# Optimization experiments

Hardware: AMD Instinct MI355X
Metric: run time of the kernel (lower is better)

Reference implementation:

```python
import jax, jax.numpy as jnp
import numpy as np

N_NODES = 1_000_000
D_IN = 128
GRAPH_STATE_DIM = 128  # node_hidden_sizes[-1] before doubling
N_GRAPHS = 4096


def setup_inputs() -> dict:
    key = jax.random.key(0)
    ks = jax.random.split(key, 10)
    s = lambda fan_in: 1.0 / np.sqrt(fan_in)
    return {
        "node_states": jax.random.normal(ks[0], (N_NODES, D_IN), dtype=jnp.float32),
        "graph_idx": jax.random.randint(ks[1], (N_NODES,), 0, N_GRAPHS),
        # MLP1: D_IN -> 64 -> 2*GRAPH_STATE_DIM
        "W1": jax.random.uniform(ks[2], (D_IN, 64), jnp.float32, -s(D_IN), s(D_IN)),
        "b1": jnp.zeros((64,), jnp.float32),
        "W2": jax.random.uniform(ks[3], (64, 2 * GRAPH_STATE_DIM), jnp.float32, -s(64), s(64)),
        "b2": jnp.zeros((2 * GRAPH_STATE_DIM,), jnp.float32),
        # MLP2: GRAPH_STATE_DIM -> 32 -> 16
        "W3": jax.random.uniform(ks[4], (GRAPH_STATE_DIM, 32), jnp.float32, -s(GRAPH_STATE_DIM), s(GRAPH_STATE_DIM)),
        "b3": jnp.zeros((32,), jnp.float32),
        "W4": jax.random.uniform(ks[5], (32, 16), jnp.float32, -s(32), s(32)),
        "b4": jnp.zeros((16,), jnp.float32),
    }


def reference(node_states, graph_idx, W1, b1, W2, b2, W3, b3, W4, b4):
    # MLP1: [N, D_IN] -> [N, 2*GRAPH_STATE_DIM]
    h = jax.nn.relu(node_states @ W1 + b1) @ W2 + b2
    gates = jax.nn.sigmoid(h[:, :GRAPH_STATE_DIM])
    gated = h[:, GRAPH_STATE_DIM:] * gates  # [N, GRAPH_STATE_DIM]
    # unsorted segment sum over graphs (n_graphs = max(graph_idx)+1 = N_GRAPHS)
    graph_states = jax.ops.segment_sum(gated, graph_idx, num_segments=N_GRAPHS)
    # MLP2: [G, GRAPH_STATE_DIM] -> [G, 16]
    out = jax.nn.relu(graph_states @ W3 + b3) @ W4 + b4
    return out
```

## Files before the change

kernel.cpp:

```cpp
#include <hip/hip_runtime.h>
#include <hip/hip_bf16.h>

#define N_NODES 1000000
#define D_IN 128
#define NG 4096
#define GSD 128
#define NGROUP_MAX 35232
#define K5_BLOCKS 8808
#define CPAD 16

typedef __attribute__((ext_vector_type(4))) float f32x4;
typedef __attribute__((ext_vector_type(8))) short bf16x8;
typedef __attribute__((ext_vector_type(4))) int i32x4;

__device__ __forceinline__ short f2bs(float f) {
    unsigned u = __float_as_uint(f);
    u += 0x7FFF + ((u >> 16) & 1);
    return (short)(u >> 16);
}

__device__ __forceinline__ int cvt_pk_bf16(float lo, float hi) {
    int r;
    asm("v_cvt_pk_bf16_f32 %0, %1, %2" : "=v"(r) : "v"(lo), "v"(hi));
    return r;
}

__device__ __forceinline__ float sigmoid_fast(float x) {
    float e = __builtin_amdgcn_exp2f(-1.44269504089f * x);
    return __builtin_amdgcn_rcpf(1.0f + e);
}

__global__ void wconv_kernel(const float* __restrict__ W1, const float* __restrict__ W2,
                             short* __restrict__ w1t, short* __restrict__ w2t) {
    int idx = blockIdx.x * 256 + threadIdx.x;
    if (idx < 8192) {
        int n = idx >> 7, rem = idx & 127, c = rem >> 3, j = rem & 7;
        int k = ((c ^ (n & 15)) << 3) | j;
        w1t[idx] = f2bs(W1[k * 64 + n]);
    } else {
        int s = idx - 8192;
        int n = s >> 6, rem = s & 63, c = rem >> 3, j = rem & 7;
        int k = ((c ^ (n & 7)) << 3) | j;
        w2t[s] = f2bs(W2[k * 256 + n]);
    }
}

__global__ void hist_kernel(const int* __restrict__ gidx, int* __restrict__ cnt) {
    __shared__ int h[NG];
    int t = threadIdx.x;
    for (int i = t; i < NG; i += 256) h[i] = 0;
    __syncthreads();
    for (int i = blockIdx.x * 256 + t; i < N_NODES; i += gridDim.x * 256)
        atomicAdd(&h[gidx[i]], 1);
    __syncthreads();
    for (int i = t; i < NG; i += 256) {
        int v = h[i];
        if (v) atomicAdd(&cnt[i * CPAD], v);
    }
}

__global__ __launch_bounds__(1024) void scan_kernel(const int* __restrict__ cnt,
                                                    int* __restrict__ poff,
                                                    int* __restrict__ ggid,
                                                    int* __restrict__ meta) {
    __shared__ int sc[1024];
    int t = threadIdx.x;
    int cc[4], c[4];
    int s = 0;
#pragma unroll
    for (int i = 0; i < 4; ++i) {
        cc[i] = cnt[(t * 4 + i) * CPAD];
        c[i] = (cc[i] + 31) & ~31;
        s += c[i];
    }
    sc[t] = s;
    __syncthreads();
    for (int off = 1; off < 1024; off <<= 1) {
        int v = (t >= off) ? sc[t - off] : 0;
        __syncthreads();
        sc[t] += v;
        __syncthreads();
    }
    if (t == 1023) meta[0] = sc[1023] >> 5;
    int base = sc[t] - s;
#pragma unroll
    for (int i = 0; i < 4; ++i) {
        int g = t * 4 + i;
        poff[g] = base;
        int ngp = c[i] >> 5;
        int gb = base >> 5;
        for (int k = 0; k < ngp; ++k) {
            int rem = cc[i] - k * 32;
            int rows = rem > 32 ? 32 : rem;
            ggid[gb + k] = (g << 6) | (rows - 1);
        }
        base += c[i];
    }
}

__global__ void scatter_kernel(const int* __restrict__ gidx, const int* __restrict__ poff,
                               int* __restrict__ cur, int* __restrict__ order) {
    int i = blockIdx.x * 256 + threadIdx.x;
    if (i >= N_NODES) return;
    int g = gidx[i];
    int p = atomicAdd(&cur[g * CPAD], 1);
    order[poff[g] + p] = i;
}

__global__ __launch_bounds__(256, 4) void main_kernel(
        const float* __restrict__ X, const short* __restrict__ w1t,
        const short* __restrict__ w2t, const float* __restrict__ b1,
        const float* __restrict__ b2, const int* __restrict__ order,
        const int* __restrict__ ggid, const int* __restrict__ meta,
        float* __restrict__ gs) {
    __shared__ __align__(16) short lds[8192];
    const int tid = threadIdx.x;
    const int wid = tid >> 6;
    const int w = (blockIdx.x << 2) + wid;
    const int lane = tid & 63;
    const int l15 = lane & 15;
    const int q = lane >> 4;
    const int ngroups = meta[0];
    const bool active = (w < ngroups);
    const int h1b = wid * 2048;

    int g = 0;
    unsigned rowmask = 0;

    if (active) {
        int enc = ggid[w];
        g = enc >> 6;
        int rows = (enc & 63) + 1;
        rowmask = (rows >= 32) ? 0xFFFFFFFFu : ((1u << rows) - 1u);
        bool v0 = l15 < rows;
        bool v1 = (16 + l15) < rows;
        int nd0r = order[w * 32 + l15];
        int nd1r = order[w * 32 + 16 + l15];
        const float* xp0 = X + (long long)(v0 ? nd0r : 0) * D_IN;
        const float* xp1 = X + (long long)(v1 ? nd1r : 0) * D_IN;

        f32x4 acc1[2][4];
#pragma unroll
        for (int mt = 0; mt < 2; ++mt)
#pragma unroll
            for (int nt = 0; nt < 4; ++nt) acc1[mt][nt] = (f32x4){0.f, 0.f, 0.f, 0.f};

        const f32x4 z = {0.f, 0.f, 0.f, 0.f};
#pragma unroll
        for (int kk = 0; kk < 4; ++kk) {
            int koff = kk * 32 + q * 8;
            f32x4 x00 = v0 ? *(const f32x4*)(xp0 + koff) : z;
            f32x4 x01 = v0 ? *(const f32x4*)(xp0 + koff + 4) : z;
            f32x4 x10 = v1 ? *(const f32x4*)(xp1 + koff) : z;
            f32x4 x11 = v1 ? *(const f32x4*)(xp1 + koff + 4) : z;
            union { bf16x8 v; int i[4]; } ua0, ua1;
            ua0.i[0] = cvt_pk_bf16(x00[0], x00[1]);
            ua0.i[1] = cvt_pk_bf16(x00[2], x00[3]);
            ua0.i[2] = cvt_pk_bf16(x01[0], x01[1]);
            ua0.i[3] = cvt_pk_bf16(x01[2], x01[3]);
            ua1.i[0] = cvt_pk_bf16(x10[0], x10[1]);
            ua1.i[1] = cvt_pk_bf16(x10[2], x10[3]);
            ua1.i[2] = cvt_pk_bf16(x11[0], x11[1]);
            ua1.i[3] = cvt_pk_bf16(x11[2], x11[3]);
            int ch = kk * 4 + q;
#pragma unroll
            for (int nt = 0; nt < 4; ++nt) {
                bf16x8 b = *(const bf16x8*)&w1t[(nt * 16 + l15) * 128 + ((ch ^ l15) << 3)];
                acc1[0][nt] = __builtin_amdgcn_mfma_f32_16x16x32_bf16(ua0.v, b, acc1[0][nt], 0, 0, 0);
                acc1[1][nt] = __builtin_amdgcn_mfma_f32_16x16x32_bf16(ua1.v, b, acc1[1][nt], 0, 0, 0);
            }
        }

#pragma unroll
        for (int nt = 0; nt < 4; ++nt) {
            float bb = b1[nt * 16 + l15];
            int c = nt * 2 + (l15 >> 3);
            int j7 = l15 & 7;
#pragma unroll
            for (int mt = 0; mt < 2; ++mt)
#pragma unroll
                for (int r = 0; r < 4; ++r) {
                    int m = mt * 16 + q * 4 + r;
                    float h = fmaxf(acc1[mt][nt][r] + bb, 0.f);
                    lds[h1b + m * 64 + ((c ^ (m & 7)) << 3) + j7] = (short)cvt_pk_bf16(h, h);
                }
        }
    }

    __syncthreads();

    if (active) {
        bf16x8 A0[2], A1[2];
#pragma unroll
        for (int ks = 0; ks < 2; ++ks) {
            int ch = ((ks * 4 + q) ^ (l15 & 7)) << 3;
            A0[ks] = *(const bf16x8*)&lds[h1b + l15 * 64 + ch];
            A1[ks] = *(const bf16x8*)&lds[h1b + (16 + l15) * 64 + ch];
        }
#pragma unroll
        for (int nt = 0; nt < 8; ++nt) {
            f32x4 aG0 = (f32x4){0.f, 0.f, 0.f, 0.f}, aG1 = aG0, aV0 = aG0, aV1 = aG0;
#pragma unroll
            for (int ks = 0; ks < 2; ++ks) {
                int ch = ((ks * 4 + q) ^ (l15 & 7)) << 3;
                bf16x8 bG = *(const bf16x8*)&w2t[(nt * 16 + l15) * 64 + ch];
                bf16x8 bV = *(const bf16x8*)&w2t[((nt + 8) * 16 + l15) * 64 + ch];
                aG0 = __builtin_amdgcn_mfma_f32_16x16x32_bf16(A0[ks], bG, aG0, 0, 0, 0);
                aG1 = __builtin_amdgcn_mfma_f32_16x16x32_bf16(A1[ks], bG, aG1, 0, 0, 0);
                aV0 = __builtin_amdgcn_mfma_f32_16x16x32_bf16(A0[ks], bV, aV0, 0, 0, 0);
                aV1 = __builtin_amdgcn_mfma_f32_16x16x32_bf16(A1[ks], bV, aV1, 0, 0, 0);
            }
            float bg = b2[nt * 16 + l15];
            float bv = b2[128 + nt * 16 + l15];
            float s = 0.f;
#pragma unroll
            for (int mt = 0; mt < 2; ++mt) {
                f32x4 aG = mt ? aG1 : aG0;
                f32x4 aV = mt ? aV1 : aV0;
#pragma unroll
                for (int r = 0; r < 4; ++r) {
                    int row = mt * 16 + q * 4 + r;
                    float gate = sigmoid_fast(aG[r] + bg);
                    float gv = gate * (aV[r] + bv);
                    s += ((rowmask >> row) & 1u) ? gv : 0.f;
                }
            }
            s += __shfl_xor(s, 16);
            s += __shfl_xor(s, 32);
            if (lane < 16) unsafeAtomicAdd(&gs[(long long)g * GSD + nt * 16 + l15], s);
        }
    }
}

__global__ void mlp2_kernel(const float* __restrict__ gs, const float* __restrict__ W3,
                            const float* __restrict__ b3, const float* __restrict__ W4,
                            const float* __restrict__ b4, float* __restrict__ out) {
    __shared__ __align__(16) float sgs[8 * 128];
    __shared__ float sh3[8 * 32];
    int t = threadIdx.x;
    int g0 = blockIdx.x * 8;
    *(f32x4*)&sgs[t * 4] = *(const f32x4*)(gs + (long long)g0 * 128 + t * 4);
    __syncthreads();
    {
        int li = t >> 5, j = t & 31;
        float acc = b3[j];
#pragma unroll 8
        for (int k = 0; k < 128; ++k) acc += sgs[li * 128 + k] * W3[k * 32 + j];
        sh3[li * 32 + j] = fmaxf(acc, 0.f);
    }
    __syncthreads();
    if (t < 128) {
        int li = t >> 4, o = t & 15;
        float acc = b4[o];
#pragma unroll
        for (int j = 0; j < 32; ++j) acc += sh3[li * 32 + j] * W4[j * 16 + o];
        out[(g0 + li) * 16 + o] = acc;
    }
}

extern "C" void kernel_launch(void* const* d_in, const int* in_sizes, int n_in,
                              void* d_out, int out_size, void* d_ws, size_t ws_size,
                              hipStream_t stream) {
    (void)in_sizes; (void)n_in; (void)out_size; (void)ws_size;
    const float* X  = (const float*)d_in[0];
    const int* gidx = (const int*)d_in[1];
    const float* W1 = (const float*)d_in[2];
    const float* b1 = (const float*)d_in[3];
    const float* W2 = (const float*)d_in[4];
    const float* b2 = (const float*)d_in[5];
    const float* W3 = (const float*)d_in[6];
    const float* b3 = (const float*)d_in[7];
    const float* W4 = (const float*)d_in[8];
    const float* b4 = (const float*)d_in[9];
    float* out = (float*)d_out;

    char* ws   = (char*)d_ws;
    float* gs  = (float*)(ws + 0);
    int* cnt   = (int*)(ws + 2097152);
    int* cur   = (int*)(ws + 2359296);
    int* poff  = (int*)(ws + 2621440);
    int* meta  = (int*)(ws + 2637824);
    short* w1t = (short*)(ws + 2637888);
    short* w2t = (short*)(ws + 2654272);
    int* ggid  = (int*)(ws + 2687040);
    int* order = (int*)(ws + 2827968);

    hipMemsetAsync(ws, 0, 2621440, stream);

    wconv_kernel<<<96, 256, 0, stream>>>(W1, W2, w1t, w2t);
    hist_kernel<<<512, 256, 0, stream>>>(gidx, cnt);
    scan_kernel<<<1, 1024, 0, stream>>>(cnt, poff, ggid, meta);
    scatter_kernel<<<(N_NODES + 255) / 256, 256, 0, stream>>>(gidx, poff, cur, order);
    main_kernel<<<K5_BLOCKS, 256, 0, stream>>>(X, w1t, w2t, b1, b2, order, ggid, meta, gs);
    mlp2_kernel<<<512, 256, 0, stream>>>(gs, W3, b3, W4, b4, out);
}
```

Baseline: 839.1 us.

## Replace global-atomic histogram and memset with per-block partial histograms

The histogram kernel now runs 64 blocks of 1024 threads with vectorized index loads and writes per-block partial counts instead of doing global atomics into a padded count array. The scan kernel sums the partials and also zeroes the scatter cursors. Zeroing of the graph-state accumulator moves into the scatter kernel, so the separate memset launch is gone. This trims launch overhead and global atomic contention on the small preprocessing stages, at the cost of a serial 64-way reduction inside the single-block scan.

```diff
diff --git a/kernel.cpp b/kernel.cpp
--- a/kernel.cpp
+++ b/kernel.cpp
@@ -8,6 +8,7 @@
 #define NGROUP_MAX 35232
 #define K5_BLOCKS 8808
 #define CPAD 16
+#define HIST_BLOCKS 64
 
 typedef __attribute__((ext_vector_type(4))) float f32x4;
 typedef __attribute__((ext_vector_type(8))) short bf16x8;
@@ -45,31 +46,40 @@
     }
 }
 
-__global__ void hist_kernel(const int* __restrict__ gidx, int* __restrict__ cnt) {
+__global__ __launch_bounds__(1024) void hist_kernel(const int* __restrict__ gidx,
+                                                    int* __restrict__ part) {
     __shared__ int h[NG];
     int t = threadIdx.x;
-    for (int i = t; i < NG; i += 256) h[i] = 0;
-    __syncthreads();
-    for (int i = blockIdx.x * 256 + t; i < N_NODES; i += gridDim.x * 256)
-        atomicAdd(&h[gidx[i]], 1);
-    __syncthreads();
-    for (int i = t; i < NG; i += 256) {
-        int v = h[i];
-        if (v) atomicAdd(&cnt[i * CPAD], v);
-    }
-}
-
-__global__ __launch_bounds__(1024) void scan_kernel(const int* __restrict__ cnt,
+    for (int i = t; i < NG; i += 1024) h[i] = 0;
+    __syncthreads();
+    const i32x4* g4 = (const i32x4*)gidx;
+    for (int i = blockIdx.x * 1024 + t; i < N_NODES / 4; i += HIST_BLOCKS * 1024) {
+        i32x4 v = g4[i];
+        atomicAdd(&h[v[0]], 1);
+        atomicAdd(&h[v[1]], 1);
+        atomicAdd(&h[v[2]], 1);
+        atomicAdd(&h[v[3]], 1);
+    }
+    __syncthreads();
+    for (int i = t; i < NG; i += 1024) part[blockIdx.x * NG + i] = h[i];
+}
+
+__global__ __launch_bounds__(1024) void scan_kernel(const int* __restrict__ part,
                                                     int* __restrict__ poff,
                                                     int* __restrict__ ggid,
-                                                    int* __restrict__ meta) {
+                                                    int* __restrict__ meta,
+                                                    int* __restrict__ cur) {
     __shared__ int sc[1024];
     int t = threadIdx.x;
+    i32x4 a4 = (i32x4){0, 0, 0, 0};
+#pragma unroll 8
+    for (int b = 0; b < HIST_BLOCKS; ++b)
+        a4 += *(const i32x4*)&part[b * NG + t * 4];
     int cc[4], c[4];
     int s = 0;
 #pragma unroll
     for (int i = 0; i < 4; ++i) {
-        cc[i] = cnt[(t * 4 + i) * CPAD];
+        cc[i] = a4[i];
         c[i] = (cc[i] + 31) & ~31;
         s += c[i];
     }
@@ -87,6 +97,7 @@
     for (int i = 0; i < 4; ++i) {
         int g = t * 4 + i;
         poff[g] = base;
+        cur[g * CPAD] = 0;
         int ngp = c[i] >> 5;
         int gb = base >> 5;
         for (int k = 0; k < ngp; ++k) {
@@ -99,8 +110,11 @@
 }
 
 __global__ void scatter_kernel(const int* __restrict__ gidx, const int* __restrict__ poff,
-                               int* __restrict__ cur, int* __restrict__ order) {
+                               int* __restrict__ cur, int* __restrict__ order,
+                               float* __restrict__ gs) {
     int i = blockIdx.x * 256 + threadIdx.x;
+    if (i < (NG * GSD) / 4)
+        *(f32x4*)&gs[i * 4] = (f32x4){0.f, 0.f, 0.f, 0.f};
     if (i >= N_NODES) return;
     int g = gidx[i];
     int p = atomicAdd(&cur[g * CPAD], 1);
@@ -276,21 +290,19 @@
 
     char* ws   = (char*)d_ws;
     float* gs  = (float*)(ws + 0);
-    int* cnt   = (int*)(ws + 2097152);
-    int* cur   = (int*)(ws + 2359296);
-    int* poff  = (int*)(ws + 2621440);
-    int* meta  = (int*)(ws + 2637824);
-    short* w1t = (short*)(ws + 2637888);
-    short* w2t = (short*)(ws + 2654272);
-    int* ggid  = (int*)(ws + 2687040);
-    int* order = (int*)(ws + 2827968);
-
-    hipMemsetAsync(ws, 0, 2621440, stream);
+    int* cur   = (int*)(ws + 2097152);
+    int* poff  = (int*)(ws + 2359296);
+    int* meta  = (int*)(ws + 2375680);
+    short* w1t = (short*)(ws + 2375744);
+    short* w2t = (short*)(ws + 2392128);
+    int* ggid  = (int*)(ws + 2424896);
+    int* part  = (int*)(ws + 2565824);
+    int* order = (int*)(ws + 3614400);
 
     wconv_kernel<<<96, 256, 0, stream>>>(W1, W2, w1t, w2t);
-    hist_kernel<<<512, 256, 0, stream>>>(gidx, cnt);
-    scan_kernel<<<1, 1024, 0, stream>>>(cnt, poff, ggid, meta);
-    scatter_kernel<<<(N_NODES + 255) / 256, 256, 0, stream>>>(gidx, poff, cur, order);
+    hist_kernel<<<HIST_BLOCKS, 1024, 0, stream>>>(gidx, part);
+    scan_kernel<<<1, 1024, 0, stream>>>(part, poff, ggid, meta, cur);
+    scatter_kernel<<<(N_NODES + 255) / 256, 256, 0, stream>>>(gidx, poff, cur, order, gs);
     main_kernel<<<K5_BLOCKS, 256, 0, stream>>>(X, w1t, w2t, b1, b2, order, ggid, meta, gs);
     mlp2_kernel<<<512, 256, 0, stream>>>(gs, W3, b3, W4, b4, out);
 }
```

Result: faster. 814.0 us (-3.0%).
